# Kernel tuning notes

Hardware: AMD Instinct MI355X
Metric: run time of the kernel (lower is better)

Reference implementation:

```python
import jax, jax.numpy as jnp
import numpy as np

B, T, D, H, E = 2, 1024, 1024, 4096, 8


def setup_inputs() -> dict:
    key = jax.random.key(0)
    ks = jax.random.split(key, 6)
    x = jax.random.normal(ks[0], (B, T, D), dtype=jnp.float32)
    padding_mask = jnp.zeros((B, T), dtype=bool)
    # Gate: Linear(D, E, bias=False) -> weight (E, D)
    Wg = jax.random.normal(ks[1], (E, D), dtype=jnp.float32) * (1.0 / np.sqrt(D))
    # Stacked expert FFN params (torch Linear layout: weight (out, in))
    W1 = jax.random.normal(ks[2], (E, H, D), dtype=jnp.float32) * (1.0 / np.sqrt(D))
    b1 = jax.random.normal(ks[3], (E, H), dtype=jnp.float32) * 0.01
    W2 = jax.random.normal(ks[4], (E, D, H), dtype=jnp.float32) * (1.0 / np.sqrt(H))
    b2 = jax.random.normal(ks[5], (E, D), dtype=jnp.float32) * 0.01
    return {"x": x, "padding_mask": padding_mask, "Wg": Wg, "W1": W1, "b1": b1, "W2": W2, "b2": b2}


def _top2_gate(xt, pm, Wg):
    # xt: (nt, D) flattened tokens, pm: (nt,) bool padding mask
    nt, ec = xt.shape[0], Wg.shape[0]
    logits = (xt @ Wg.T).astype(jnp.float32)            # use_fp32=True
    gate_value = jax.nn.softmax(logits, axis=-1)        # (nt, E)
    gate_value = jnp.where(pm[:, None], 0.0, gate_value)
    top2_idx = jax.lax.top_k(gate_value, 2)[1]          # (nt, 2)
    keep = jax.nn.one_hot(top2_idx, ec, dtype=bool).any(axis=1)  # (nt, E) True at top1/top2
    gate_weights = jnp.where(keep, gate_value, 0.0)
    s = gate_weights.sum(axis=1, keepdims=True)
    s = jnp.where(s == 0.0, 1.0, s)
    gate_weights = gate_weights / s
    # load-balance loss: fraction of top-1 assignments vs mean gate prob per expert
    nt_real = (~pm).sum().astype(jnp.float32)
    top1_counts = (jax.nn.one_hot(top2_idx[:, 0], ec, dtype=jnp.float32)
                   * (~pm)[:, None].astype(jnp.float32)).sum(axis=0)  # (E,)
    lb_loss = ec * ((top1_counts / nt_real) * (gate_value.sum(axis=0) / nt_real)).sum()
    return lb_loss, gate_weights, gate_value


def reference(x, padding_mask, Wg, W1, b1, W2, b2):
    Bx, Tx, Dx = x.shape
    xt = x.reshape(-1, Dx)                   # (nt, D)
    pm = padding_mask.reshape(-1)            # (nt,)
    lb_loss, gw, gate_value = _top2_gate(xt, pm, Wg)
    gw = gw.astype(x.dtype)                  # (nt, E)
    # Expert FFNs (dense over experts; routing weights are zero except top-2)
    h = jax.nn.relu(jnp.einsum('nd,ehd->neh', xt, W1) + b1)   # (nt, E, H)
    y = jnp.einsum('neh,edh->ned', h, W2) + b2                # (nt, E, D)
    out = jnp.einsum('ne,ned->nd', gw, y).reshape(Bx, Tx, Dx)
    return out, gate_value, lb_loss
```

## Files before the change

### kernel.cpp

```cpp
#include <hip/hip_runtime.h>
#include <hip/hip_bf16.h>
#include <stdint.h>


#define NTOK 2048
#define DDIM 1024
#define HDIM 4096
#define NEXP 8
#define KSPLIT 2
#define CONVB 1024
#define GATEB (NTOK / 4)
#define ZEROB 512

typedef float  f32x4  __attribute__((ext_vector_type(4)));
typedef __bf16 bf16x8 __attribute__((ext_vector_type(8)));
typedef __bf16 bf16x4 __attribute__((ext_vector_type(4)));

typedef const __attribute__((address_space(1))) void g1_t;
typedef __attribute__((address_space(3))) void l3_t;
__device__ __forceinline__ void gld16(const void* g, void* l) {
  __builtin_amdgcn_global_load_lds((g1_t*)g, (l3_t*)l, 16, 0, 0);
}

__global__ void init_kernel(int* fill) {
  int t = threadIdx.x;
  if (t < NEXP) fill[t] = 0;
}

__device__ __forceinline__ void conv_body(int bid, const float* __restrict__ src,
                                          __bf16* __restrict__ dst, long n8) {
  long i = (long)bid * 256 + threadIdx.x;
  long stride = (long)CONVB * 256;
  for (; i < n8; i += stride) {
    f32x4 a = ((const f32x4*)src)[2 * i];
    f32x4 b = ((const f32x4*)src)[2 * i + 1];
    bf16x8 o;
#pragma unroll
    for (int q = 0; q < 4; ++q) { o[q] = (__bf16)a[q]; o[q + 4] = (__bf16)b[q]; }
    ((bf16x8*)dst)[i] = o;
  }
}

__device__ __forceinline__ void zero_body(int bid, float* __restrict__ y, long n4) {
  long i = (long)bid * 256 + threadIdx.x;
  long stride = (long)ZEROB * 256;
  for (; i < n4; i += stride) ((f32x4*)y)[i] = (f32x4){0.f, 0.f, 0.f, 0.f};
}

__device__ __forceinline__ void gate_body(int bid, const float* __restrict__ x,
                                          const unsigned char* __restrict__ pmask,
                                          const float* __restrict__ Wg,
                                          float* __restrict__ gate_out,
                                          int* __restrict__ tix, float* __restrict__ twt,
                                          __bf16* __restrict__ xbf) {
  int wave = threadIdx.x >> 6, lane = threadIdx.x & 63;
  int t = bid * 4 + wave;
  const f32x4* x4 = (const f32x4*)(x + (size_t)t * DDIM);
  const f32x4* w4 = (const f32x4*)Wg;
  bf16x4* xb4 = (bf16x4*)(xbf + (size_t)t * DDIM);
  float acc[NEXP];
#pragma unroll
  for (int e = 0; e < NEXP; ++e) acc[e] = 0.f;
#pragma unroll
  for (int i = 0; i < 4; ++i) {
    f32x4 xv = x4[i * 64 + lane];
    bf16x4 xo;
#pragma unroll
    for (int q = 0; q < 4; ++q) xo[q] = (__bf16)xv[q];
    xb4[i * 64 + lane] = xo;
#pragma unroll
    for (int e = 0; e < NEXP; ++e) {
      f32x4 wv = w4[e * 256 + i * 64 + lane];
      acc[e] += xv[0]*wv[0] + xv[1]*wv[1] + xv[2]*wv[2] + xv[3]*wv[3];
    }
  }
#pragma unroll
  for (int e = 0; e < NEXP; ++e) {
    float v = acc[e];
#pragma unroll
    for (int off = 32; off > 0; off >>= 1) v += __shfl_xor(v, off, 64);
    acc[e] = v;
  }
  if (lane == 0) {
    bool pm = pmask[t] != 0;
    float m = acc[0];
#pragma unroll
    for (int e = 1; e < NEXP; ++e) m = fmaxf(m, acc[e]);
    float g[NEXP]; float s = 0.f;
#pragma unroll
    for (int e = 0; e < NEXP; ++e) { g[e] = expf(acc[e] - m); s += g[e]; }
    float inv = 1.f / s;
#pragma unroll
    for (int e = 0; e < NEXP; ++e) g[e] *= inv;
    if (pm) {
#pragma unroll
      for (int e = 0; e < NEXP; ++e) g[e] = 0.f;
    }
    int i1 = 0;
#pragma unroll
    for (int e = 1; e < NEXP; ++e) if (g[e] > g[i1]) i1 = e;
    int i2 = -1;
#pragma unroll
    for (int e = 0; e < NEXP; ++e) if (e != i1 && (i2 < 0 || g[e] > g[i2])) i2 = e;
    float w1 = g[i1], w2 = g[i2], ss = w1 + w2;
    if (ss == 0.f) ss = 1.f;
    w1 /= ss; w2 /= ss;
#pragma unroll
    for (int e = 0; e < NEXP; ++e) gate_out[(size_t)t * NEXP + e] = g[e];
    tix[2*t] = i1; tix[2*t+1] = i2;
    twt[2*t] = w1; twt[2*t+1] = w2;
  }
}

__global__ __launch_bounds__(256)
void preA_kernel(const float* __restrict__ x, const unsigned char* __restrict__ pmask,
                 const float* __restrict__ Wg, float* __restrict__ gate_out,
                 int* __restrict__ tix, float* __restrict__ twt,
                 __bf16* __restrict__ xbf, const float* __restrict__ W1,
                 __bf16* __restrict__ w1bf, float* __restrict__ out)
{
  int bid = blockIdx.x;
  if (bid < CONVB) { conv_body(bid, W1, w1bf, (long)NEXP * HDIM * DDIM / 8); return; }
  bid -= CONVB;
  if (bid < GATEB) { gate_body(bid, x, pmask, Wg, gate_out, tix, twt, xbf); return; }
  bid -= GATEB;
  zero_body(bid, out, (long)NTOK * DDIM / 4);
}

__global__ __launch_bounds__(1024)
void stats_kernel(const float* __restrict__ gate_out, const int* __restrict__ tix,
                  const unsigned char* __restrict__ pmask,
                  int* __restrict__ ecount, int* __restrict__ offs,
                  float* __restrict__ lb_out)
{
  int tid = threadIdx.x, lane = tid & 63, wv = tid >> 6;
  float lg[NEXP]; float lt1[NEXP]; int lec[NEXP]; float ln = 0.f;
#pragma unroll
  for (int e = 0; e < NEXP; ++e) { lg[e] = 0.f; lt1[e] = 0.f; lec[e] = 0; }
#pragma unroll
  for (int it = 0; it < NTOK / 1024; ++it) {
    int t = tid + it * 1024;
    f32x4 g0 = ((const f32x4*)(gate_out + (size_t)t * NEXP))[0];
    f32x4 g1 = ((const f32x4*)(gate_out + (size_t)t * NEXP))[1];
    lg[0] += g0[0]; lg[1] += g0[1]; lg[2] += g0[2]; lg[3] += g0[3];
    lg[4] += g1[0]; lg[5] += g1[1]; lg[6] += g1[2]; lg[7] += g1[3];
    if (!pmask[t]) {
      int i1 = tix[2*t], i2 = tix[2*t+1];
      lt1[i1] += 1.f; lec[i1] += 1; lec[i2] += 1; ln += 1.f;
    }
  }
#pragma unroll
  for (int e = 0; e < NEXP; ++e) {
#pragma unroll
    for (int off = 32; off > 0; off >>= 1) {
      lg[e]  += __shfl_xor(lg[e],  off, 64);
      lt1[e] += __shfl_xor(lt1[e], off, 64);
      lec[e] += __shfl_xor(lec[e], off, 64);
    }
  }
#pragma unroll
  for (int off = 32; off > 0; off >>= 1) ln += __shfl_xor(ln, off, 64);
  __shared__ float sg[16][NEXP], st[16][NEXP], sn[16];
  __shared__ int   se[16][NEXP];
  if (lane == 0) {
#pragma unroll
    for (int e = 0; e < NEXP; ++e) { sg[wv][e] = lg[e]; st[wv][e] = lt1[e]; se[wv][e] = lec[e]; }
    sn[wv] = ln;
  }
  __syncthreads();
  if (tid == 0) {
    float G[NEXP] = {0}, T1[NEXP] = {0}; int EC[NEXP] = {0}; float N = 0.f;
    for (int w = 0; w < 16; ++w) {
      N += sn[w];
#pragma unroll
      for (int e = 0; e < NEXP; ++e) { G[e] += sg[w][e]; T1[e] += st[w][e]; EC[e] += se[w][e]; }
    }
    int o = 0;
    for (int e = 0; e < NEXP; ++e) { ecount[e] = EC[e]; offs[e] = o; o += EC[e]; }
    if (N <= 0.f) N = 1.f;
    float lb = 0.f;
    for (int e = 0; e < NEXP; ++e) lb += (T1[e] / N) * (G[e] / N);
    lb_out[0] = (float)NEXP * lb;
  }
}

__global__ __launch_bounds__(256)
void compact_kernel(const unsigned char* __restrict__ pmask, const int* __restrict__ tix,
                    const float* __restrict__ twt, const int* __restrict__ offs,
                    int* __restrict__ fill, int* __restrict__ tok_list,
                    float* __restrict__ wgt_list)
{
  int t = blockIdx.x * 256 + threadIdx.x;
  int lane = threadIdx.x & 63;
  bool pm = pmask[t] != 0;
#pragma unroll
  for (int j = 0; j < 2; ++j) {
    int e = pm ? -1 : tix[2*t + j];
    int pos = -1;
#pragma unroll
    for (int ex = 0; ex < NEXP; ++ex) {
      unsigned long long mask = __ballot(e == ex);
      if (mask) {
        int leader = (int)(__ffsll((long long)mask) - 1);
        int base = 0;
        if (lane == leader) base = atomicAdd(&fill[ex], (int)__popcll(mask));
        base = __shfl(base, leader, 64);
        if (e == ex)
          pos = offs[ex] + base + (int)__popcll(mask & ((1ull << lane) - 1ull));
      }
    }
    if (e >= 0) { tok_list[pos] = t; wgt_list[pos] = twt[2*t + j]; }
  }
}


__device__ __forceinline__ void gemm1_body(int bid, const __bf16* __restrict__ xbf,
                                           const __bf16* __restrict__ w1bf,
                                           const float* __restrict__ b1,
                                           const int* __restrict__ ecount,
                                           const int* __restrict__ offs,
                                           const int* __restrict__ tok_list,
                                           __bf16* __restrict__ hbuf)
{
  const int NTILE = HDIM / 128;
  const int MTILE = NTOK / 128;
  int e = bid / (MTILE * NTILE);
  int rem = bid % (MTILE * NTILE);
  int mt = rem / NTILE, nt = rem % NTILE;
  int cnt = ecount[e];
  if (mt * 128 >= cnt) return;
  int off = offs[e];

  __shared__ __bf16 As[3][128 * 32];
  __shared__ __bf16 Bs[3][128 * 32];

  int tid = threadIdx.x, lane = tid & 63, wave = tid >> 6;
  int wm = wave >> 1, wn = wave & 1;

  const __bf16* aP[2];
  const __bf16* bP[2];
#pragma unroll
  for (int c = 0; c < 2; ++c) {
    int row = c * 64 + (tid >> 2);
    int cd = (tid & 3) ^ ((row >> 1) & 3);
    int mrow = mt * 128 + row;
    int tok = tok_list[off + ((mrow < cnt) ? mrow : 0)];
    aP[c] = xbf + (size_t)tok * DDIM + cd * 8;
    bP[c] = w1bf + (size_t)e * HDIM * DDIM + (size_t)(nt * 128 + row) * DDIM + cd * 8;
  }
  int cg = ((lane >> 4) ^ ((lane >> 1) & 3)) << 3;

  f32x4 acc[4][4];
#pragma unroll
  for (int m = 0; m < 4; ++m)
#pragma unroll
    for (int n = 0; n < 4; ++n) acc[m][n] = (f32x4){0.f, 0.f, 0.f, 0.f};

  const int NIT = DDIM / 32;
#pragma unroll
  for (int pt = 0; pt < 2; ++pt)
#pragma unroll
    for (int c = 0; c < 2; ++c) {
      gld16(aP[c] + pt * 32, &As[pt][(c * 64 + wave * 16) * 32]);
      gld16(bP[c] + pt * 32, &Bs[pt][(c * 64 + wave * 16) * 32]);
    }

  for (int it = 0; it < NIT; ++it) {
    int cur = it % 3;
    if (it + 1 < NIT) asm volatile("s_waitcnt vmcnt(4)" ::: "memory");
    else              asm volatile("s_waitcnt vmcnt(0)" ::: "memory");
    __builtin_amdgcn_s_barrier();
    __builtin_amdgcn_sched_barrier(0);
    if (it + 2 < NIT) {
      int nb = (it + 2) % 3;
      int k0 = (it + 2) * 32;
#pragma unroll
      for (int c = 0; c < 2; ++c) {
        gld16(aP[c] + k0, &As[nb][(c * 64 + wave * 16) * 32]);
        gld16(bP[c] + k0, &Bs[nb][(c * 64 + wave * 16) * 32]);
      }
    }
    bf16x8 af[4], bfr[4];
#pragma unroll
    for (int m = 0; m < 4; ++m) af[m]  = *(const bf16x8*)&As[cur][(wm*64 + m*16 + (lane & 15)) * 32 + cg];
#pragma unroll
    for (int n = 0; n < 4; ++n) bfr[n] = *(const bf16x8*)&Bs[cur][(wn*64 + n*16 + (lane & 15)) * 32 + cg];
#pragma unroll
    for (int m = 0; m < 4; ++m)
#pragma unroll
      for (int n = 0; n < 4; ++n)
        acc[m][n] = __builtin_amdgcn_mfma_f32_16x16x32_bf16(af[m], bfr[n], acc[m][n], 0, 0, 0);
  }

#pragma unroll
  for (int n = 0; n < 4; ++n) {
    int col = nt * 128 + wn * 64 + n * 16 + (lane & 15);
    float bias = b1[e * HDIM + col];
#pragma unroll
    for (int m = 0; m < 4; ++m) {
#pragma unroll
      for (int j = 0; j < 4; ++j) {
        int mr = mt * 128 + wm * 64 + m * 16 + ((lane >> 4) << 2) + j;
        if (mr < cnt) {
          float v = fmaxf(acc[m][n][j] + bias, 0.f);
          hbuf[(size_t)(off + mr) * HDIM + col] = (__bf16)v;
        }
      }
    }
  }
}

__global__ __launch_bounds__(256)
void gemm1u_kernel(const __bf16* __restrict__ xbf, const __bf16* __restrict__ w1bf,
                   const float* __restrict__ b1, const int* __restrict__ ecount,
                   const int* __restrict__ offs, const int* __restrict__ tok_list,
                   __bf16* __restrict__ hbuf, const float* __restrict__ W2,
                   __bf16* __restrict__ w2bf)
{
  if (blockIdx.x < CONVB) { conv_body(blockIdx.x, W2, w2bf, (long)NEXP * DDIM * HDIM / 8); return; }
  gemm1_body(blockIdx.x - CONVB, xbf, w1bf, b1, ecount, offs, tok_list, hbuf);
}

__global__ __launch_bounds__(256)
void gemm1_kernel(const __bf16* __restrict__ xbf, const __bf16* __restrict__ w1bf,
                  const float* __restrict__ b1, const int* __restrict__ ecount,
                  const int* __restrict__ offs, const int* __restrict__ tok_list,
                  __bf16* __restrict__ hbuf)
{
  gemm1_body(blockIdx.x, xbf, w1bf, b1, ecount, offs, tok_list, hbuf);
}

__global__ __launch_bounds__(256)
void conv_kernel(const float* __restrict__ src, __bf16* __restrict__ dst, long n8)
{
  conv_body(blockIdx.x, src, dst, n8);
}

__global__ __launch_bounds__(256)
void gemm2_kernel(const __bf16* __restrict__ hbuf, const __bf16* __restrict__ w2bf,
                  const float* __restrict__ b2, const int* __restrict__ ecount,
                  const int* __restrict__ offs, const int* __restrict__ tok_list,
                  const float* __restrict__ wgt_list, float* __restrict__ out)
{
  const int NTILE = DDIM / 128;
  const int MTILE = NTOK / 128;
  int bid = blockIdx.x;
  int e = bid / (MTILE * NTILE * KSPLIT);
  int rem = bid % (MTILE * NTILE * KSPLIT);
  int mt = rem / (NTILE * KSPLIT);
  int rem2 = rem % (NTILE * KSPLIT);
  int nt = rem2 / KSPLIT, kc = rem2 % KSPLIT;
  int cnt = ecount[e];
  if (mt * 128 >= cnt) return;
  int off = offs[e];

  __shared__ __bf16 As[3][128 * 32];
  __shared__ __bf16 Bs[3][128 * 32];

  int tid = threadIdx.x, lane = tid & 63, wave = tid >> 6;
  int wm = wave >> 1, wn = wave & 1;

  const __bf16* aP[2];
  const __bf16* bP[2];
#pragma unroll
  for (int c = 0; c < 2; ++c) {
    int row = c * 64 + (tid >> 2);
    int cd = (tid & 3) ^ ((row >> 1) & 3);
    aP[c] = hbuf + (size_t)(off + mt * 128 + row) * HDIM + cd * 8;
    bP[c] = w2bf + (size_t)e * DDIM * HDIM + (size_t)(nt * 128 + row) * HDIM + cd * 8;
  }
  int cg = ((lane >> 4) ^ ((lane >> 1) & 3)) << 3;

  f32x4 acc[4][4];
#pragma unroll
  for (int m = 0; m < 4; ++m)
#pragma unroll
    for (int n = 0; n < 4; ++n) acc[m][n] = (f32x4){0.f, 0.f, 0.f, 0.f};

  const int KCH = HDIM / KSPLIT;
  const int NIT = KCH / 32;
  int kbeg = kc * KCH;
#pragma unroll
  for (int pt = 0; pt < 2; ++pt)
#pragma unroll
    for (int c = 0; c < 2; ++c) {
      gld16(aP[c] + kbeg + pt * 32, &As[pt][(c * 64 + wave * 16) * 32]);
      gld16(bP[c] + kbeg + pt * 32, &Bs[pt][(c * 64 + wave * 16) * 32]);
    }

  for (int it = 0; it < NIT; ++it) {
    int cur = it % 3;
    if (it + 1 < NIT) asm volatile("s_waitcnt vmcnt(4)" ::: "memory");
    else              asm volatile("s_waitcnt vmcnt(0)" ::: "memory");
    __builtin_amdgcn_s_barrier();
    __builtin_amdgcn_sched_barrier(0);
    if (it + 2 < NIT) {
      int nb = (it + 2) % 3;
      int k0 = kbeg + (it + 2) * 32;
#pragma unroll
      for (int c = 0; c < 2; ++c) {
        gld16(aP[c] + k0, &As[nb][(c * 64 + wave * 16) * 32]);
        gld16(bP[c] + k0, &Bs[nb][(c * 64 + wave * 16) * 32]);
      }
    }
    bf16x8 af[4], bfr[4];
#pragma unroll
    for (int m = 0; m < 4; ++m) af[m]  = *(const bf16x8*)&As[cur][(wm*64 + m*16 + (lane & 15)) * 32 + cg];
#pragma unroll
    for (int n = 0; n < 4; ++n) bfr[n] = *(const bf16x8*)&Bs[cur][(wn*64 + n*16 + (lane & 15)) * 32 + cg];
#pragma unroll
    for (int m = 0; m < 4; ++m)
#pragma unroll
      for (int n = 0; n < 4; ++n)
        acc[m][n] = __builtin_amdgcn_mfma_f32_16x16x32_bf16(af[m], bfr[n], acc[m][n], 0, 0, 0);
  }

  float b2v[4];
#pragma unroll
  for (int n = 0; n < 4; ++n) {
    int col = nt * 128 + wn * 64 + n * 16 + (lane & 15);
    b2v[n] = (kc == 0) ? b2[e * DDIM + col] : 0.f;
  }
#pragma unroll
  for (int m = 0; m < 4; ++m) {
#pragma unroll
    for (int j = 0; j < 4; ++j) {
      int mr = mt * 128 + wm * 64 + m * 16 + ((lane >> 4) << 2) + j;
      if (mr >= cnt) continue;
      int slot = off + mr;
      int tok = tok_list[slot];
      float w = wgt_list[slot];
      float* obase = out + (size_t)tok * DDIM;
#pragma unroll
      for (int n = 0; n < 4; ++n) {
        int col = nt * 128 + wn * 64 + n * 16 + (lane & 15);
        atomicAdd(obase + col, w * (acc[m][n][j] + b2v[n]));
      }
    }
  }
}

extern "C" void kernel_launch(void* const* d_in, const int* in_sizes, int n_in,
                              void* d_out, int out_size, void* d_ws, size_t ws_size,
                              hipStream_t stream)
{
  const float* x  = (const float*)d_in[0];
  const unsigned char* pm = (const unsigned char*)d_in[1];
  const float* Wg = (const float*)d_in[2];
  const float* W1 = (const float*)d_in[3];
  const float* b1 = (const float*)d_in[4];
  const float* W2 = (const float*)d_in[5];
  const float* b2 = (const float*)d_in[6];
  float* out = (float*)d_out;
  float* gate_out = out + (size_t)NTOK * DDIM;
  float* lb_out = gate_out + (size_t)NTOK * NEXP;

  char* w = (char*)d_ws;
  int*   ecount   = (int*)(w + 0);
  int*   offs     = (int*)(w + 64);
  int*   fill     = (int*)(w + 128);
  int*   tix      = (int*)(w + 512);
  float* twt      = (float*)(w + 512 + 16384);
  int*   tok_list = (int*)(w + 512 + 32768);
  float* wgt_list = (float*)(w + 512 + 49152);
  uintptr_t p = ((uintptr_t)(w + 512 + 65536) + 255) & ~(uintptr_t)255;
  __bf16* xbf  = (__bf16*)p;
  p += (size_t)NTOK * DDIM * 2;
  __bf16* w1bf = (__bf16*)p;
  p += (size_t)NEXP * HDIM * DDIM * 2;
  __bf16* hbuf = (__bf16*)p;
  p += (size_t)(2 * NTOK + 128) * HDIM * 2;
  __bf16* w2bf_sep = (__bf16*)p;
  size_t need = (size_t)((char*)(w2bf_sep + (size_t)NEXP * DDIM * HDIM) - w);
  bool overlap = (ws_size >= need);
  __bf16* w2bf = overlap ? w2bf_sep : w1bf;

  init_kernel<<<1, 64, 0, stream>>>(fill);
  preA_kernel<<<CONVB + GATEB + ZEROB, 256, 0, stream>>>(x, pm, Wg, gate_out, tix, twt, xbf, W1, w1bf, out);
  stats_kernel<<<1, 1024, 0, stream>>>(gate_out, tix, pm, ecount, offs, lb_out);
  compact_kernel<<<NTOK / 256, 256, 0, stream>>>(pm, tix, twt, offs, fill, tok_list, wgt_list);
  if (overlap) {
    gemm1u_kernel<<<CONVB + NEXP * (NTOK / 128) * (HDIM / 128), 256, 0, stream>>>(
        xbf, w1bf, b1, ecount, offs, tok_list, hbuf, W2, w2bf);
  } else {
    gemm1_kernel<<<NEXP * (NTOK / 128) * (HDIM / 128), 256, 0, stream>>>(
        xbf, w1bf, b1, ecount, offs, tok_list, hbuf);
    conv_kernel<<<CONVB, 256, 0, stream>>>(W2, w2bf, (long)NEXP * DDIM * HDIM / 8);
  }
  gemm2_kernel<<<NEXP * (NTOK / 128) * (DDIM / 128) * KSPLIT, 256, 0, stream>>>(
      hbuf, w2bf, b2, ecount, offs, tok_list, wgt_list, out);
}
```

Measured before the change: 286.9 us.

## Widen GEMM N-tiles to 256, drop init kernel, unfuse W2 conversion

Both expert GEMMs now use 128x256 output tiles, with each wave computing 64x128 via 4x8 MFMA accumulators. This is meant to reuse the A tile more and halve the number of blocks. The fill-counter reset moves into stats_kernel, which removes one launch. The W2 fp32-to-bf16 conversion is no longer co-scheduled inside the gemm1 launch and runs as a separate kernel afterwards, giving up that overlap. The larger tiles raise register and LDS use and may lower occupancy, and gemm2 now has fewer blocks to spread across the CUs.

Result: slower. 308.4 us (+7.5%).

```diff
diff --git a/kernel.cpp b/kernel.cpp
--- a/kernel.cpp
+++ b/kernel.cpp
@@ -20,11 +20,6 @@
 typedef __attribute__((address_space(3))) void l3_t;
 __device__ __forceinline__ void gld16(const void* g, void* l) {
   __builtin_amdgcn_global_load_lds((g1_t*)g, (l3_t*)l, 16, 0, 0);
-}
-
-__global__ void init_kernel(int* fill) {
-  int t = threadIdx.x;
-  if (t < NEXP) fill[t] = 0;
 }
 
 __device__ __forceinline__ void conv_body(int bid, const float* __restrict__ src,
@@ -127,11 +122,17 @@
   zero_body(bid, out, (long)NTOK * DDIM / 4);
 }
 
+__global__ __launch_bounds__(256)
+void conv_kernel(const float* __restrict__ src, __bf16* __restrict__ dst, long n8)
+{
+  conv_body(blockIdx.x, src, dst, n8);
+}
+
 __global__ __launch_bounds__(1024)
 void stats_kernel(const float* __restrict__ gate_out, const int* __restrict__ tix,
                   const unsigned char* __restrict__ pmask,
                   int* __restrict__ ecount, int* __restrict__ offs,
-                  float* __restrict__ lb_out)
+                  int* __restrict__ fill, float* __restrict__ lb_out)
 {
   int tid = threadIdx.x, lane = tid & 63, wv = tid >> 6;
   float lg[NEXP]; float lt1[NEXP]; int lec[NEXP]; float ln = 0.f;
@@ -176,7 +177,7 @@
       for (int e = 0; e < NEXP; ++e) { G[e] += sg[w][e]; T1[e] += st[w][e]; EC[e] += se[w][e]; }
     }
     int o = 0;
-    for (int e = 0; e < NEXP; ++e) { ecount[e] = EC[e]; offs[e] = o; o += EC[e]; }
+    for (int e = 0; e < NEXP; ++e) { ecount[e] = EC[e]; offs[e] = o; o += EC[e]; fill[e] = 0; }
     if (N <= 0.f) N = 1.f;
     float lb = 0.f;
     for (int e = 0; e < NEXP; ++e) lb += (T1[e] / N) * (G[e] / N);
@@ -214,31 +215,29 @@
 }
 
 
-__device__ __forceinline__ void gemm1_body(int bid, const __bf16* __restrict__ xbf,
-                                           const __bf16* __restrict__ w1bf,
-                                           const float* __restrict__ b1,
-                                           const int* __restrict__ ecount,
-                                           const int* __restrict__ offs,
-                                           const int* __restrict__ tok_list,
-                                           __bf16* __restrict__ hbuf)
-{
-  const int NTILE = HDIM / 128;
-  const int MTILE = NTOK / 128;
-  int e = bid / (MTILE * NTILE);
-  int rem = bid % (MTILE * NTILE);
-  int mt = rem / NTILE, nt = rem % NTILE;
+__global__ __launch_bounds__(256)
+void gemm1_kernel(const __bf16* __restrict__ xbf, const __bf16* __restrict__ w1bf,
+                  const float* __restrict__ b1, const int* __restrict__ ecount,
+                  const int* __restrict__ offs, const int* __restrict__ tok_list,
+                  __bf16* __restrict__ hbuf)
+{
+  const int NT1 = HDIM / 256;
+  const int MT1 = NTOK / 128;
+  int bid = blockIdx.x;
+  int e = bid / (MT1 * NT1);
+  int rem = bid % (MT1 * NT1);
+  int mt = rem / NT1, nt = rem % NT1;
   int cnt = ecount[e];
   if (mt * 128 >= cnt) return;
   int off = offs[e];
 
   __shared__ __bf16 As[3][128 * 32];
-  __shared__ __bf16 Bs[3][128 * 32];
+  __shared__ __bf16 Bs[3][256 * 32];
 
   int tid = threadIdx.x, lane = tid & 63, wave = tid >> 6;
   int wm = wave >> 1, wn = wave & 1;
 
   const __bf16* aP[2];
-  const __bf16* bP[2];
 #pragma unroll
   for (int c = 0; c < 2; ++c) {
     int row = c * 64 + (tid >> 2);
@@ -246,28 +245,34 @@
     int mrow = mt * 128 + row;
     int tok = tok_list[off + ((mrow < cnt) ? mrow : 0)];
     aP[c] = xbf + (size_t)tok * DDIM + cd * 8;
-    bP[c] = w1bf + (size_t)e * HDIM * DDIM + (size_t)(nt * 128 + row) * DDIM + cd * 8;
+  }
+  const __bf16* bP[4];
+#pragma unroll
+  for (int c = 0; c < 4; ++c) {
+    int row = c * 64 + (tid >> 2);
+    int cd = (tid & 3) ^ ((row >> 1) & 3);
+    bP[c] = w1bf + (size_t)e * HDIM * DDIM + (size_t)(nt * 256 + row) * DDIM + cd * 8;
   }
   int cg = ((lane >> 4) ^ ((lane >> 1) & 3)) << 3;
 
-  f32x4 acc[4][4];
+  f32x4 acc[4][8];
 #pragma unroll
   for (int m = 0; m < 4; ++m)
 #pragma unroll
-    for (int n = 0; n < 4; ++n) acc[m][n] = (f32x4){0.f, 0.f, 0.f, 0.f};
+    for (int n = 0; n < 8; ++n) acc[m][n] = (f32x4){0.f, 0.f, 0.f, 0.f};
 
   const int NIT = DDIM / 32;
 #pragma unroll
-  for (int pt = 0; pt < 2; ++pt)
-#pragma unroll
-    for (int c = 0; c < 2; ++c) {
-      gld16(aP[c] + pt * 32, &As[pt][(c * 64 + wave * 16) * 32]);
-      gld16(bP[c] + pt * 32, &Bs[pt][(c * 64 + wave * 16) * 32]);
-    }
+  for (int pt = 0; pt < 2; ++pt) {
+#pragma unroll
+    for (int c = 0; c < 2; ++c) gld16(aP[c] + pt * 32, &As[pt][(c * 64 + wave * 16) * 32]);
+#pragma unroll
+    for (int c = 0; c < 4; ++c) gld16(bP[c] + pt * 32, &Bs[pt][(c * 64 + wave * 16) * 32]);
+  }
 
   for (int it = 0; it < NIT; ++it) {
     int cur = it % 3;
-    if (it + 1 < NIT) asm volatile("s_waitcnt vmcnt(4)" ::: "memory");
+    if (it + 1 < NIT) asm volatile("s_waitcnt vmcnt(6)" ::: "memory");
     else              asm volatile("s_waitcnt vmcnt(0)" ::: "memory");
     __builtin_amdgcn_s_barrier();
     __builtin_amdgcn_sched_barrier(0);
@@ -275,26 +280,25 @@
       int nb = (it + 2) % 3;
       int k0 = (it + 2) * 32;
 #pragma unroll
-      for (int c = 0; c < 2; ++c) {
-        gld16(aP[c] + k0, &As[nb][(c * 64 + wave * 16) * 32]);
-        gld16(bP[c] + k0, &Bs[nb][(c * 64 + wave * 16) * 32]);
-      }
-    }
-    bf16x8 af[4], bfr[4];
+      for (int c = 0; c < 2; ++c) gld16(aP[c] + k0, &As[nb][(c * 64 + wave * 16) * 32]);
+#pragma unroll
+      for (int c = 0; c < 4; ++c) gld16(bP[c] + k0, &Bs[nb][(c * 64 + wave * 16) * 32]);
+    }
+    bf16x8 af[4], bfr[8];
 #pragma unroll
     for (int m = 0; m < 4; ++m) af[m]  = *(const bf16x8*)&As[cur][(wm*64 + m*16 + (lane & 15)) * 32 + cg];
 #pragma unroll
-    for (int n = 0; n < 4; ++n) bfr[n] = *(const bf16x8*)&Bs[cur][(wn*64 + n*16 + (lane & 15)) * 32 + cg];
+    for (int n = 0; n < 8; ++n) bfr[n] = *(const bf16x8*)&Bs[cur][(wn*128 + n*16 + (lane & 15)) * 32 + cg];
 #pragma unroll
     for (int m = 0; m < 4; ++m)
 #pragma unroll
-      for (int n = 0; n < 4; ++n)
+      for (int n = 0; n < 8; ++n)
         acc[m][n] = __builtin_amdgcn_mfma_f32_16x16x32_bf16(af[m], bfr[n], acc[m][n], 0, 0, 0);
   }
 
 #pragma unroll
-  for (int n = 0; n < 4; ++n) {
-    int col = nt * 128 + wn * 64 + n * 16 + (lane & 15);
+  for (int n = 0; n < 8; ++n) {
+    int col = nt * 256 + wn * 128 + n * 16 + (lane & 15);
     float bias = b1[e * HDIM + col];
 #pragma unroll
     for (int m = 0; m < 4; ++m) {
@@ -311,86 +315,65 @@
 }
 
 __global__ __launch_bounds__(256)
-void gemm1u_kernel(const __bf16* __restrict__ xbf, const __bf16* __restrict__ w1bf,
-                   const float* __restrict__ b1, const int* __restrict__ ecount,
-                   const int* __restrict__ offs, const int* __restrict__ tok_list,
-                   __bf16* __restrict__ hbuf, const float* __restrict__ W2,
-                   __bf16* __restrict__ w2bf)
-{
-  if (blockIdx.x < CONVB) { conv_body(blockIdx.x, W2, w2bf, (long)NEXP * DDIM * HDIM / 8); return; }
-  gemm1_body(blockIdx.x - CONVB, xbf, w1bf, b1, ecount, offs, tok_list, hbuf);
-}
-
-__global__ __launch_bounds__(256)
-void gemm1_kernel(const __bf16* __restrict__ xbf, const __bf16* __restrict__ w1bf,
-                  const float* __restrict__ b1, const int* __restrict__ ecount,
-                  const int* __restrict__ offs, const int* __restrict__ tok_list,
-                  __bf16* __restrict__ hbuf)
-{
-  gemm1_body(blockIdx.x, xbf, w1bf, b1, ecount, offs, tok_list, hbuf);
-}
-
-__global__ __launch_bounds__(256)
-void conv_kernel(const float* __restrict__ src, __bf16* __restrict__ dst, long n8)
-{
-  conv_body(blockIdx.x, src, dst, n8);
-}
-
-__global__ __launch_bounds__(256)
 void gemm2_kernel(const __bf16* __restrict__ hbuf, const __bf16* __restrict__ w2bf,
                   const float* __restrict__ b2, const int* __restrict__ ecount,
                   const int* __restrict__ offs, const int* __restrict__ tok_list,
                   const float* __restrict__ wgt_list, float* __restrict__ out)
 {
-  const int NTILE = DDIM / 128;
-  const int MTILE = NTOK / 128;
+  const int NT2 = DDIM / 256;
+  const int MT2 = NTOK / 128;
   int bid = blockIdx.x;
-  int e = bid / (MTILE * NTILE * KSPLIT);
-  int rem = bid % (MTILE * NTILE * KSPLIT);
-  int mt = rem / (NTILE * KSPLIT);
-  int rem2 = rem % (NTILE * KSPLIT);
+  int e = bid / (MT2 * NT2 * KSPLIT);
+  int rem = bid % (MT2 * NT2 * KSPLIT);
+  int mt = rem / (NT2 * KSPLIT);
+  int rem2 = rem % (NT2 * KSPLIT);
   int nt = rem2 / KSPLIT, kc = rem2 % KSPLIT;
   int cnt = ecount[e];
   if (mt * 128 >= cnt) return;
   int off = offs[e];
 
   __shared__ __bf16 As[3][128 * 32];
-  __shared__ __bf16 Bs[3][128 * 32];
+  __shared__ __bf16 Bs[3][256 * 32];
 
   int tid = threadIdx.x, lane = tid & 63, wave = tid >> 6;
   int wm = wave >> 1, wn = wave & 1;
 
   const __bf16* aP[2];
-  const __bf16* bP[2];
 #pragma unroll
   for (int c = 0; c < 2; ++c) {
     int row = c * 64 + (tid >> 2);
     int cd = (tid & 3) ^ ((row >> 1) & 3);
     aP[c] = hbuf + (size_t)(off + mt * 128 + row) * HDIM + cd * 8;
-    bP[c] = w2bf + (size_t)e * DDIM * HDIM + (size_t)(nt * 128 + row) * HDIM + cd * 8;
+  }
+  const __bf16* bP[4];
+#pragma unroll
+  for (int c = 0; c < 4; ++c) {
+    int row = c * 64 + (tid >> 2);
+    int cd = (tid & 3) ^ ((row >> 1) & 3);
+    bP[c] = w2bf + (size_t)e * DDIM * HDIM + (size_t)(nt * 256 + row) * HDIM + cd * 8;
   }
   int cg = ((lane >> 4) ^ ((lane >> 1) & 3)) << 3;
 
-  f32x4 acc[4][4];
+  f32x4 acc[4][8];
 #pragma unroll
   for (int m = 0; m < 4; ++m)
 #pragma unroll
-    for (int n = 0; n < 4; ++n) acc[m][n] = (f32x4){0.f, 0.f, 0.f, 0.f};
+    for (int n = 0; n < 8; ++n) acc[m][n] = (f32x4){0.f, 0.f, 0.f, 0.f};
 
   const int KCH = HDIM / KSPLIT;
   const int NIT = KCH / 32;
   int kbeg = kc * KCH;
 #pragma unroll
-  for (int pt = 0; pt < 2; ++pt)
-#pragma unroll
-    for (int c = 0; c < 2; ++c) {
-      gld16(aP[c] + kbeg + pt * 32, &As[pt][(c * 64 + wave * 16) * 32]);
-      gld16(bP[c] + kbeg + pt * 32, &Bs[pt][(c * 64 + wave * 16) * 32]);
-    }
+  for (int pt = 0; pt < 2; ++pt) {
+#pragma unroll
+    for (int c = 0; c < 2; ++c) gld16(aP[c] + kbeg + pt * 32, &As[pt][(c * 64 + wave * 16) * 32]);
+#pragma unroll
+    for (int c = 0; c < 4; ++c) gld16(bP[c] + kbeg + pt * 32, &Bs[pt][(c * 64 + wave * 16) * 32]);
+  }
 
   for (int it = 0; it < NIT; ++it) {
     int cur = it % 3;
-    if (it + 1 < NIT) asm volatile("s_waitcnt vmcnt(4)" ::: "memory");
+    if (it + 1 < NIT) asm volatile("s_waitcnt vmcnt(6)" ::: "memory");
     else              asm volatile("s_waitcnt vmcnt(0)" ::: "memory");
     __builtin_amdgcn_s_barrier();
     __builtin_amdgcn_sched_barrier(0);
@@ -398,27 +381,26 @@
       int nb = (it + 2) % 3;
       int k0 = kbeg + (it + 2) * 32;
 #pragma unroll
-      for (int c = 0; c < 2; ++c) {
-        gld16(aP[c] + k0, &As[nb][(c * 64 + wave * 16) * 32]);
-        gld16(bP[c] + k0, &Bs[nb][(c * 64 + wave * 16) * 32]);
-      }
-    }
-    bf16x8 af[4], bfr[4];
+      for (int c = 0; c < 2; ++c) gld16(aP[c] + k0, &As[nb][(c * 64 + wave * 16) * 32]);
+#pragma unroll
+      for (int c = 0; c < 4; ++c) gld16(bP[c] + k0, &Bs[nb][(c * 64 + wave * 16) * 32]);
+    }
+    bf16x8 af[4], bfr[8];
 #pragma unroll
     for (int m = 0; m < 4; ++m) af[m]  = *(const bf16x8*)&As[cur][(wm*64 + m*16 + (lane & 15)) * 32 + cg];
 #pragma unroll
-    for (int n = 0; n < 4; ++n) bfr[n] = *(const bf16x8*)&Bs[cur][(wn*64 + n*16 + (lane & 15)) * 32 + cg];
+    for (int n = 0; n < 8; ++n) bfr[n] = *(const bf16x8*)&Bs[cur][(wn*128 + n*16 + (lane & 15)) * 32 + cg];
 #pragma unroll
     for (int m = 0; m < 4; ++m)
 #pragma unroll
-      for (int n = 0; n < 4; ++n)
+      for (int n = 0; n < 8; ++n)
         acc[m][n] = __builtin_amdgcn_mfma_f32_16x16x32_bf16(af[m], bfr[n], acc[m][n], 0, 0, 0);
   }
 
-  float b2v[4];
-#pragma unroll
-  for (int n = 0; n < 4; ++n) {
-    int col = nt * 128 + wn * 64 + n * 16 + (lane & 15);
+  float b2v[8];
+#pragma unroll
+  for (int n = 0; n < 8; ++n) {
+    int col = nt * 256 + wn * 128 + n * 16 + (lane & 15);
     b2v[n] = (kc == 0) ? b2[e * DDIM + col] : 0.f;
   }
 #pragma unroll
@@ -432,8 +414,8 @@
       float w = wgt_list[slot];
       float* obase = out + (size_t)tok * DDIM;
 #pragma unroll
-      for (int n = 0; n < 4; ++n) {
-        int col = nt * 128 + wn * 64 + n * 16 + (lane & 15);
+      for (int n = 0; n < 8; ++n) {
+        int col = nt * 256 + wn * 128 + n * 16 + (lane & 15);
         atomicAdd(obase + col, w * (acc[m][n][j] + b2v[n]));
       }
     }
@@ -472,21 +454,14 @@
   p += (size_t)(2 * NTOK + 128) * HDIM * 2;
   __bf16* w2bf_sep = (__bf16*)p;
   size_t need = (size_t)((char*)(w2bf_sep + (size_t)NEXP * DDIM * HDIM) - w);
-  bool overlap = (ws_size >= need);
-  __bf16* w2bf = overlap ? w2bf_sep : w1bf;
-
-  init_kernel<<<1, 64, 0, stream>>>(fill);
+  __bf16* w2bf = (ws_size >= need) ? w2bf_sep : w1bf;
+
   preA_kernel<<<CONVB + GATEB + ZEROB, 256, 0, stream>>>(x, pm, Wg, gate_out, tix, twt, xbf, W1, w1bf, out);
-  stats_kernel<<<1, 1024, 0, stream>>>(gate_out, tix, pm, ecount, offs, lb_out);
+  stats_kernel<<<1, 1024, 0, stream>>>(gate_out, tix, pm, ecount, offs, fill, lb_out);
   compact_kernel<<<NTOK / 256, 256, 0, stream>>>(pm, tix, twt, offs, fill, tok_list, wgt_list);
-  if (overlap) {
-    gemm1u_kernel<<<CONVB + NEXP * (NTOK / 128) * (HDIM / 128), 256, 0, stream>>>(
-        xbf, w1bf, b1, ecount, offs, tok_list, hbuf, W2, w2bf);
-  } else {
-    gemm1_kernel<<<NEXP * (NTOK / 128) * (HDIM / 128), 256, 0, stream>>>(
-        xbf, w1bf, b1, ecount, offs, tok_list, hbuf);
-    conv_kernel<<<CONVB, 256, 0, stream>>>(W2, w2bf, (long)NEXP * DDIM * HDIM / 8);
-  }
-  gemm2_kernel<<<NEXP * (NTOK / 128) * (DDIM / 128) * KSPLIT, 256, 0, stream>>>(
+  gemm1_kernel<<<NEXP * (NTOK / 128) * (HDIM / 256), 256, 0, stream>>>(
+      xbf, w1bf, b1, ecount, offs, tok_list, hbuf);
+  conv_kernel<<<CONVB, 256, 0, stream>>>(W2, w2bf, (long)NEXP * DDIM * HDIM / 8);
+  gemm2_kernel<<<NEXP * (NTOK / 128) * (DDIM / 256) * KSPLIT, 256, 0, stream>>>(
       hbuf, w2bf, b2, ecount, offs, tok_list, wgt_list, out);
 }
```
